# Kernel tuning notes

Hardware: AMD Instinct MI355X
Metric: run time of the kernel (lower is better)

Reference implementation:

```python
import math
import jax, jax.numpy as jnp
import numpy as np

D_MODEL = 1024
NUM_HEADS = 16
D_HEAD = D_MODEL // NUM_HEADS  # 64
K_S = 32  # sparse top-k keys kept per query
B, N = 2, 2048


def setup_inputs() -> dict:
    key = jax.random.key(0)
    ks = jax.random.split(key, 9)
    s = 1.0 / math.sqrt(D_MODEL)
    return {
        "x": jax.random.normal(ks[0], (B, N, D_MODEL), dtype=jnp.float32),
        "Wq": jax.random.normal(ks[1], (D_MODEL, D_MODEL), dtype=jnp.float32) * s,
        "bq": jnp.zeros((D_MODEL,), dtype=jnp.float32),
        "Wk": jax.random.normal(ks[2], (D_MODEL, D_MODEL), dtype=jnp.float32) * s,
        "bk": jnp.zeros((D_MODEL,), dtype=jnp.float32),
        "Wv": jax.random.normal(ks[3], (D_MODEL, D_MODEL), dtype=jnp.float32) * s,
        "bv": jnp.zeros((D_MODEL,), dtype=jnp.float32),
        "Wo": jax.random.normal(ks[4], (D_MODEL, D_MODEL), dtype=jnp.float32) * s,
        "bo": jnp.zeros((D_MODEL,), dtype=jnp.float32),
    }


def _attn(x, Wq, bq, Wk, bk, Wv, bv, Wo, bo):
    b, n, _ = x.shape
    # projections (torch Linear: y = x W^T + b)
    q = (x @ Wq.T + bq).reshape(b, n, NUM_HEADS, D_HEAD).transpose(0, 2, 1, 3)
    k = (x @ Wk.T + bk).reshape(b, n, NUM_HEADS, D_HEAD).transpose(0, 2, 1, 3)
    v = (x @ Wv.T + bv).reshape(b, n, NUM_HEADS, D_HEAD).transpose(0, 2, 1, 3)
    # full scores [b, H, n, n]
    scores = jnp.einsum("bhqd,bhkd->bhqk", q, k) / math.sqrt(D_HEAD)
    # causal mask (triu above diagonal -> -inf)
    causal = jnp.triu(jnp.ones((n, n), dtype=bool), k=1)
    neg_inf = jnp.array(-jnp.inf, dtype=scores.dtype)
    scores = jnp.where(causal, neg_inf, scores)
    # sparse top-k: keep only K_S largest scores per query row
    vals, idx = jax.lax.top_k(scores, K_S)
    masked = jnp.full_like(scores, -jnp.inf)
    masked = jnp.put_along_axis(masked, idx, vals, axis=-1, inplace=False)
    attn = jax.nn.softmax(masked, axis=-1)  # dropout p=0.0 -> identity
    out = jnp.einsum("bhqk,bhkd->bhqd", attn, v)
    out = out.transpose(0, 2, 1, 3).reshape(b, n, D_MODEL)
    y = out @ Wo.T + bo
    return y, attn.mean(axis=1)


def reference(x, Wq, bq, Wk, bk, Wv, bv, Wo, bo):
    return _attn(x, Wq, bq, Wk, bk, Wv, bv, Wo, bo)
```

## Files before the change

### kernel.cpp

```cpp
#include <hip/hip_runtime.h>
#include <hip/hip_bf16.h>
#include <math.h>

#define BATCH   2
#define NTOK    2048
#define DMODEL  1024
#define HEADS   16
#define DHEAD   64
#define KSEL    32
#define MROWS   (BATCH * NTOK)
#define NBLK8   (NTOK / 8)
#define TPW     8

typedef short     bf16x8 __attribute__((ext_vector_type(8)));
typedef float     f32x4  __attribute__((ext_vector_type(4)));
typedef unsigned short ushort_t;
typedef unsigned long long u64;

#define GLOAD_LDS16(g, l) \
    __builtin_amdgcn_global_load_lds((const __attribute__((address_space(1))) void*)(g), \
                                     (__attribute__((address_space(3))) void*)(l), 16, 0, 0)

__device__ __forceinline__ ushort_t f2bf(float f) {
    unsigned u = __float_as_uint(f);
    unsigned r = (u + 0x7FFFu + ((u >> 16) & 1u)) >> 16;
    return (ushort_t)r;
}
__device__ __forceinline__ float bf2f(ushort_t h) {
    return __uint_as_float(((unsigned)h) << 16);
}

__global__ __launch_bounds__(256) void conv_split(const float* __restrict__ in,
                                                  ushort_t* __restrict__ hi,
                                                  ushort_t* __restrict__ lo, int n)
{
    const int i = (blockIdx.x * 256 + threadIdx.x) * 4;
    if (i + 3 < n) {
        const float4 v = *(const float4*)(in + i);
        ushort4 ph, pl;
        ph.x = f2bf(v.x); pl.x = f2bf(v.x - bf2f(ph.x));
        ph.y = f2bf(v.y); pl.y = f2bf(v.y - bf2f(ph.y));
        ph.z = f2bf(v.z); pl.z = f2bf(v.z - bf2f(ph.z));
        ph.w = f2bf(v.w); pl.w = f2bf(v.w - bf2f(ph.w));
        *(ushort4*)(hi + i) = ph;
        *(ushort4*)(lo + i) = pl;
    }
}

__global__ __launch_bounds__(256) void zero_fill(float* __restrict__ p, int n4)
{
    const int i = blockIdx.x * 256 + threadIdx.x;
    if (i < n4) ((float4*)p)[i] = (float4){0.f, 0.f, 0.f, 0.f};
}

__device__ __forceinline__ unsigned mono_key(float f) {
    const unsigned u = __float_as_uint(f);
    return (u ^ (unsigned)(((int)u >> 31) | 0x80000000)) + 1u;
}
__device__ __forceinline__ float unmono(unsigned m) {
    const unsigned u = m - 1u;
    return __uint_as_float(u ^ (unsigned)(((int)(~u) >> 31) | 0x80000000));
}

__global__ __launch_bounds__(256, 2) void gemm_split_mfma(const ushort_t* __restrict__ Ahi,
                                                          const ushort_t* __restrict__ Alo,
                                                          const ushort_t* __restrict__ Bhi,
                                                          const ushort_t* __restrict__ Blo,
                                                          const float* __restrict__ bias,
                                                          float* __restrict__ out,
                                                          ushort_t* __restrict__ oh,
                                                          ushort_t* __restrict__ om,
                                                          ushort_t* __restrict__ ol,
                                                          int mode)
{
    __shared__ ushort_t smem[2 * 12288];

    const int tid  = threadIdx.x;
    const int wave = tid >> 6;
    const int lane = tid & 63;
    const int fr   = lane & 15;
    const int k8   = lane >> 4;
    const int m0 = blockIdx.x * 128;
    const int n0 = blockIdx.y * 64;

    f32x4 acc[2][4];
#pragma unroll
    for (int i = 0; i < 2; ++i)
#pragma unroll
        for (int j = 0; j < 4; ++j) acc[i][j] = (f32x4){0.f, 0.f, 0.f, 0.f};

#define STAGE(bufsel, k0v) do {                                                \
        ushort_t* dst_ = smem + (bufsel) * 12288;                              \
        _Pragma("unroll")                                                      \
        for (int i_ = 0; i_ < 2; ++i_) {                                       \
            const int c_ = i_ * 256 + tid;                                     \
            const int row_ = c_ >> 2;                                          \
            const int g_ = (c_ & 3) ^ ((row_ >> 1) & 3);                       \
            const size_t ga_ = (size_t)(m0 + row_) * DMODEL + (k0v) + g_ * 8;  \
            GLOAD_LDS16(Ahi + ga_, dst_ + (size_t)c_ * 8);                     \
            GLOAD_LDS16(Alo + ga_, dst_ + 4096 + (size_t)c_ * 8);              \
        }                                                                      \
        {                                                                      \
            const int c_ = tid;                                                \
            const int row_ = c_ >> 2;                                          \
            const int g_ = (c_ & 3) ^ ((row_ >> 1) & 3);                       \
            const size_t gb_ = (size_t)(n0 + row_) * DMODEL + (k0v) + g_ * 8;  \
            GLOAD_LDS16(Bhi + gb_, dst_ + 8192 + (size_t)c_ * 8);              \
            GLOAD_LDS16(Blo + gb_, dst_ + 10240 + (size_t)c_ * 8);             \
        }                                                                      \
    } while (0)

    STAGE(0, 0);
    int cur = 0;

    for (int k0 = 0; k0 < DMODEL; k0 += 32) {
        __syncthreads();
        if (k0 + 32 < DMODEL) STAGE(cur ^ 1, k0 + 32);

        const ushort_t* buf = smem + cur * 12288;
        bf16x8 afh[2], afl[2], bfh[4], bfl[4];
#pragma unroll
        for (int mi = 0; mi < 2; ++mi) {
            const int r = wave * 32 + mi * 16 + fr;
            const int ro = r * 32 + (k8 ^ ((r >> 1) & 3)) * 8;
            afh[mi] = *(const bf16x8*)(buf + ro);
            afl[mi] = *(const bf16x8*)(buf + 4096 + ro);
        }
#pragma unroll
        for (int ni = 0; ni < 4; ++ni) {
            const int r = ni * 16 + fr;
            const int ro = r * 32 + (k8 ^ ((r >> 1) & 3)) * 8;
            bfh[ni] = *(const bf16x8*)(buf + 8192 + ro);
            bfl[ni] = *(const bf16x8*)(buf + 10240 + ro);
        }

#pragma unroll
        for (int mi = 0; mi < 2; ++mi)
#pragma unroll
            for (int ni = 0; ni < 4; ++ni) {
                acc[mi][ni] = __builtin_amdgcn_mfma_f32_16x16x32_bf16(afh[mi], bfl[ni], acc[mi][ni], 0, 0, 0);
                acc[mi][ni] = __builtin_amdgcn_mfma_f32_16x16x32_bf16(afl[mi], bfh[ni], acc[mi][ni], 0, 0, 0);
                acc[mi][ni] = __builtin_amdgcn_mfma_f32_16x16x32_bf16(afh[mi], bfh[ni], acc[mi][ni], 0, 0, 0);
            }
        cur ^= 1;
    }
#undef STAGE

#pragma unroll
    for (int ni = 0; ni < 4; ++ni) {
        const int o = n0 + ni * 16 + (lane & 15);
        const float bv = bias[o];
#pragma unroll
        for (int mi = 0; mi < 2; ++mi) {
#pragma unroll
            for (int reg = 0; reg < 4; ++reg) {
                const int m = m0 + wave * 32 + mi * 16 + ((lane >> 4) << 2) + reg;
                const float v = acc[mi][ni][reg] + bv;
                if (mode == 0) {
                    out[(size_t)m * DMODEL + o] = v;
                } else {
                    const int bb = m >> 11;
                    const int n  = m & 2047;
                    const int hd = o >> 6;
                    const int d  = o & 63;
                    const size_t off = (((size_t)(bb * HEADS + hd)) * NTOK + n) * DHEAD + d;
                    if (mode == 1) {
                        out[off] = v;
                    } else {
                        const ushort_t h1 = f2bf(v);
                        const float r1 = v - bf2f(h1);
                        const ushort_t m1 = f2bf(r1);
                        const ushort_t l1 = f2bf(r1 - bf2f(m1));
                        oh[off] = h1; om[off] = m1; ol[off] = l1;
                    }
                }
            }
        }
    }
}

__global__ __launch_bounds__(256, 3) void score_mfma(const ushort_t* __restrict__ Qh,
                                                     const ushort_t* __restrict__ Qm,
                                                     const ushort_t* __restrict__ Ql,
                                                     const ushort_t* __restrict__ Kh,
                                                     const ushort_t* __restrict__ Km,
                                                     const ushort_t* __restrict__ Kl,
                                                     unsigned* __restrict__ S,
                                                     unsigned* __restrict__ Smax,
                                                     int q0, int QC)
{
    const int ks = blockIdx.x;
    const int qt = blockIdx.y;
    const int bh = blockIdx.z;
    const int qbase = q0 + qt * 128;
    const int ktmax = ((qbase + 127) >> 6) + 1;
    const int kt0 = ks * TPW;
    if (kt0 >= ktmax) return;
    const int kt1 = (kt0 + TPW < ktmax) ? (kt0 + TPW) : ktmax;

    __shared__ ushort_t smem[24576];

    const int tid  = threadIdx.x;
    const int wave = tid >> 6;
    const int lane = tid & 63;
    const int l15  = lane & 15;
    const int l4   = lane >> 4;

    const size_t qgbase = ((size_t)bh * NTOK + qbase) * DHEAD;

    {
        const ushort_t* Qp0 = Qh; const ushort_t* Qp1 = Qm; const ushort_t* Qp2 = Ql;
#pragma unroll
        for (int i = 0; i < 4; ++i) {
            const int c = i * 256 + tid;
            const int row = c >> 3;
            const int g = (c & 7) ^ (row & 7);
            const size_t goff = qgbase + (size_t)row * DHEAD + g * 8;
            GLOAD_LDS16(Qp0 + goff, smem + 0 * 8192 + (size_t)c * 8);
            GLOAD_LDS16(Qp1 + goff, smem + 1 * 8192 + (size_t)c * 8);
            GLOAD_LDS16(Qp2 + goff, smem + 2 * 8192 + (size_t)c * 8);
        }
    }
    __syncthreads();

    bf16x8 qf[3][2][2];
#pragma unroll
    for (int p = 0; p < 3; ++p)
#pragma unroll
        for (int j = 0; j < 2; ++j) {
            const int r = wave * 32 + j * 16 + l15;
#pragma unroll
            for (int h = 0; h < 2; ++h) {
                const int slot = (h * 4 + l4) ^ (r & 7);
                qf[p][j][h] = *(const bf16x8*)(smem + p * 8192 + (size_t)(r * 8 + slot) * 8);
            }
        }
    __syncthreads();

#define STAGE_K(bufsel, ktv) do {                                              \
        const size_t kg_ = ((size_t)bh * NTOK + (ktv) * 64) * DHEAD;           \
        _Pragma("unroll")                                                      \
        for (int i_ = 0; i_ < 2; ++i_) {                                       \
            const int c_ = i_ * 256 + tid;                                     \
            const int row_ = c_ >> 3;                                          \
            const int g_ = (c_ & 7) ^ (row_ & 7);                              \
            const size_t goff_ = kg_ + (size_t)row_ * DHEAD + g_ * 8;          \
            ushort_t* dst_ = smem + (bufsel) * 12288 + (size_t)c_ * 8;         \
            GLOAD_LDS16(Kh + goff_, dst_ + 0 * 4096);                          \
            GLOAD_LDS16(Km + goff_, dst_ + 1 * 4096);                          \
            GLOAD_LDS16(Kl + goff_, dst_ + 2 * 4096);                          \
        }                                                                      \
    } while (0)

    STAGE_K(0, kt0);
    int cur = 0;

    const size_t srowQ = (size_t)bh * QC;

    for (int kt = kt0; kt < kt1; ++kt) {
        __syncthreads();
        if (kt + 1 < kt1) STAGE_K(cur ^ 1, kt + 1);

        f32x4 acc[4][2];
#pragma unroll
        for (int m = 0; m < 4; ++m)
#pragma unroll
            for (int j = 0; j < 2; ++j) acc[m][j] = (f32x4){0.f, 0.f, 0.f, 0.f};

        const ushort_t* kb = smem + cur * 12288;
#pragma unroll
        for (int h = 0; h < 2; ++h) {
            bf16x8 kf[4];
#pragma unroll
            for (int m = 0; m < 4; ++m) {
                const int r = m * 16 + l15;
                const int slot = (h * 4 + l4) ^ (r & 7);
                kf[m] = *(const bf16x8*)(kb + 0 * 4096 + (size_t)(r * 8 + slot) * 8);
            }
#pragma unroll
            for (int m = 0; m < 4; ++m)
#pragma unroll
                for (int j = 0; j < 2; ++j) {
                    acc[m][j] = __builtin_amdgcn_mfma_f32_16x16x32_bf16(kf[m], qf[2][j][h], acc[m][j], 0, 0, 0);
                    acc[m][j] = __builtin_amdgcn_mfma_f32_16x16x32_bf16(kf[m], qf[1][j][h], acc[m][j], 0, 0, 0);
                    acc[m][j] = __builtin_amdgcn_mfma_f32_16x16x32_bf16(kf[m], qf[0][j][h], acc[m][j], 0, 0, 0);
                }
#pragma unroll
            for (int m = 0; m < 4; ++m) {
                const int r = m * 16 + l15;
                const int slot = (h * 4 + l4) ^ (r & 7);
                kf[m] = *(const bf16x8*)(kb + 1 * 4096 + (size_t)(r * 8 + slot) * 8);
            }
#pragma unroll
            for (int m = 0; m < 4; ++m)
#pragma unroll
                for (int j = 0; j < 2; ++j) {
                    acc[m][j] = __builtin_amdgcn_mfma_f32_16x16x32_bf16(kf[m], qf[1][j][h], acc[m][j], 0, 0, 0);
                    acc[m][j] = __builtin_amdgcn_mfma_f32_16x16x32_bf16(kf[m], qf[0][j][h], acc[m][j], 0, 0, 0);
                }
#pragma unroll
            for (int m = 0; m < 4; ++m) {
                const int r = m * 16 + l15;
                const int slot = (h * 4 + l4) ^ (r & 7);
                kf[m] = *(const bf16x8*)(kb + 2 * 4096 + (size_t)(r * 8 + slot) * 8);
            }
#pragma unroll
            for (int m = 0; m < 4; ++m)
#pragma unroll
                for (int j = 0; j < 2; ++j)
                    acc[m][j] = __builtin_amdgcn_mfma_f32_16x16x32_bf16(kf[m], qf[0][j][h], acc[m][j], 0, 0, 0);
        }

#pragma unroll
        for (int j = 0; j < 2; ++j) {
            const int qrow  = wave * 32 + j * 16 + l15;
            const int qlrow = qt * 128 + qrow;
            const int qglob = qbase + qrow;
            const size_t srow = (srowQ + qlrow) * NTOK;
            const size_t mrow = (srowQ + qlrow) * NBLK8;
#pragma unroll
            for (int m = 0; m < 4; ++m) {
                const int kcol0 = kt * 64 + m * 16 + (l4 << 2);
                uint4 kv;
                kv.x = mono_key(acc[m][j][0] * 0.125f);
                kv.y = mono_key(acc[m][j][1] * 0.125f);
                kv.z = mono_key(acc[m][j][2] * 0.125f);
                kv.w = mono_key(acc[m][j][3] * 0.125f);
                *(uint4*)(S + srow + kcol0) = kv;
                unsigned cm = (kcol0     <= qglob) ? kv.x : 0u;
                unsigned t;
                t = (kcol0 + 1 <= qglob) ? kv.y : 0u; cm = (t > cm) ? t : cm;
                t = (kcol0 + 2 <= qglob) ? kv.z : 0u; cm = (t > cm) ? t : cm;
                t = (kcol0 + 3 <= qglob) ? kv.w : 0u; cm = (t > cm) ? t : cm;
                const unsigned o = __shfl_xor(cm, 16, 64);
                cm = (o > cm) ? o : cm;
                if ((lane & 16) == 0) {
                    const int gblk = kt * 8 + m * 2 + (lane >> 5);
                    Smax[mrow + gblk] = cm;
                }
            }
        }
        cur ^= 1;
    }
#undef STAGE_K
}

__global__ __launch_bounds__(256) void select_v6(const unsigned* __restrict__ S,
                                                 const unsigned* __restrict__ Smax,
                                                 const float* __restrict__ V,
                                                 float* __restrict__ ctx,
                                                 float* __restrict__ attn,
                                                 int q0, int QC)
{
    __shared__ int   sBlkAll[4][KSEL];
    __shared__ int   sIdxAll[4][KSEL];
    __shared__ float sEAll[4][KSEL];

    const int lane = threadIdx.x & 63;
    const int wave = threadIdx.x >> 6;
    const int ql = blockIdx.x;
    const int b  = blockIdx.y >> 2;
    const int hg = blockIdx.y & 3;
    const int h  = hg * 4 + wave;
    const int q  = q0 + ql;
    const int L  = q + 1;
    const int nsel = (L < KSEL) ? L : KSEL;
    const int nb = (L + 7) >> 3;

    const size_t bhx = (size_t)(b * HEADS + h);
    const unsigned* Srow = S + (bhx * QC + ql) * NTOK;
    const unsigned* Mrow = Smax + (bhx * QC + ql) * NBLK8;
    const float* Vb   = V + bhx * NTOK * DHEAD;
    float* ctxRow  = ctx + (((size_t)(b * NTOK + q)) * HEADS + h) * DHEAD;
    float* attnRow = attn + ((size_t)(b * NTOK + q)) * NTOK;
    int*   sBlk = sBlkAll[wave];
    int*   sIdx = sIdxAll[wave];
    float* sE   = sEAll[wave];

    const uint4 bm4 = *(const uint4*)(Mrow + lane * 4);
    unsigned bmax[4] = {bm4.x, bm4.y, bm4.z, bm4.w};
#pragma unroll
    for (int s = 0; s < 4; ++s)
        if (lane * 4 + s >= nb) bmax[s] = 0u;

    unsigned gmax = bmax[0];
    gmax = (bmax[1] > gmax) ? bmax[1] : gmax;
    gmax = (bmax[2] > gmax) ? bmax[2] : gmax;
    gmax = (bmax[3] > gmax) ? bmax[3] : gmax;
#pragma unroll
    for (int d = 1; d < 64; d <<= 1) {
        const unsigned o = __shfl_xor(gmax, d, 64);
        gmax = (o > gmax) ? o : gmax;
    }
    const float vmax = unmono(gmax);

    unsigned selb = 0u;
    unsigned blkLo = 1u;
    int nselb;
    if (nb <= KSEL) {
        nselb = nb;
#pragma unroll
        for (int s = 0; s < 4; ++s)
            if (lane * 4 + s < nb) selb |= 1u << s;
    } else {
        nselb = KSEL;
        unsigned lo = 1u, hi = gmax >> 16;
        while (lo < hi) {
            const unsigned mid = lo + ((hi - lo + 1u) >> 1);
            const unsigned midk = mid << 16;
            int cnt = 0;
#pragma unroll
            for (int s = 0; s < 4; ++s)
                cnt += __popcll(__ballot(bmax[s] >= midk));
            if (cnt >= KSEL) lo = mid; else hi = mid - 1u;
        }
        blkLo = lo;
        const unsigned Tkb = lo << 16;
        const unsigned Gkb = Tkb | 0xFFFFu;
        int cge = 0, cgt = 0;
#pragma unroll
        for (int s = 0; s < 4; ++s) {
            cge += __popcll(__ballot(bmax[s] >= Tkb));
            cgt += __popcll(__ballot(bmax[s] > Gkb));
        }
        if (cge == KSEL) {
#pragma unroll
            for (int s = 0; s < 4; ++s)
                selb |= (bmax[s] >= Tkb) ? (1u << s) : 0u;
        } else {
            unsigned bmb = 0u;
#pragma unroll
            for (int s = 0; s < 4; ++s) {
                selb |= (bmax[s] > Gkb) ? (1u << s) : 0u;
                bmb  |= (bmax[s] >= Tkb && bmax[s] <= Gkb) ? (1u << s) : 0u;
            }
            int k_tie = KSEL - cgt;
            while (k_tie > 0) {
                u64 best = 0;
                unsigned bmm = bmb;
                while (bmm) {
                    const int s = __builtin_ctz(bmm);
                    bmm &= bmm - 1u;
                    const unsigned gblk = (unsigned)(lane * 4 + s);
                    const u64 k = ((u64)bmax[s] << 32) | (unsigned)~gblk;
                    if (k > best) best = k;
                }
                u64 bb = best;
#pragma unroll
                for (int d = 1; d < 64; d <<= 1) {
                    const u64 o = __shfl_xor(bb, d, 64);
                    bb = (o > bb) ? o : bb;
                }
                const unsigned gblk = ~(unsigned)bb;
                if (lane == (int)(gblk >> 2)) {
                    const unsigned bit = 1u << (gblk & 3u);
                    selb |= bit;
                    bmb &= ~bit;
                }
                --k_tie;
            }
        }
    }

    {
        const int cb = __popc(selb);
        int pfxb = cb;
#pragma unroll
        for (int d = 1; d < 64; d <<= 1) {
            const int t = __shfl_up(pfxb, d, 64);
            if (lane >= d) pfxb += t;
        }
        pfxb -= cb;
        unsigned mskb = selb;
        int posb = pfxb;
        while (mskb) {
            const int s = __builtin_ctz(mskb);
            mskb &= mskb - 1u;
            sBlk[posb++] = lane * 4 + s;
        }
    }
    __asm volatile("s_waitcnt lgkmcnt(0)" ::: "memory");

    const int NC = nselb * 8;
    unsigned km[4];
    int idx[4];
#pragma unroll
    for (int c = 0; c < 4; ++c) {
        const int t = c * 64 + lane;
        unsigned m = 0u;
        int j = 0;
        if (t < NC) {
            const int blk = sBlk[t >> 3];
            j = blk * 8 + (t & 7);
            if (j < L) m = Srow[j];
        }
        km[c] = m;
        idx[c] = j;
    }

    unsigned lo = blkLo, hi = gmax >> 16;
    while (lo < hi) {
        const unsigned mid = lo + ((hi - lo + 1u) >> 1);
        const unsigned midk = mid << 16;
        int cnt = 0;
#pragma unroll
        for (int c = 0; c < 4; ++c)
            cnt += __popcll(__ballot(km[c] >= midk));
        if (cnt >= nsel) lo = mid; else hi = mid - 1u;
    }
    const unsigned Tk = lo << 16;
    const unsigned Gk = Tk | 0xFFFFu;

    int cnt_ge = 0, cnt_gt = 0;
#pragma unroll
    for (int c = 0; c < 4; ++c) {
        cnt_ge += __popcll(__ballot(km[c] >= Tk));
        cnt_gt += __popcll(__ballot(km[c] > Gk));
    }

    unsigned selmask = 0u;
    if (cnt_ge == nsel) {
#pragma unroll
        for (int c = 0; c < 4; ++c)
            selmask |= (km[c] >= Tk) ? (1u << c) : 0u;
    } else {
        unsigned bmask = 0u;
#pragma unroll
        for (int c = 0; c < 4; ++c) {
            selmask |= (km[c] > Gk) ? (1u << c) : 0u;
            bmask   |= (km[c] >= Tk && km[c] <= Gk) ? (1u << c) : 0u;
        }
        int k_tie = nsel - cnt_gt;
        while (k_tie > 0) {
            u64 best = 0;
            unsigned bmm = bmask;
            while (bmm) {
                const int c = __builtin_ctz(bmm);
                bmm &= bmm - 1u;
                const int t = c * 64 + lane;
                const u64 k = ((u64)km[c] << 32) |
                              ((u64)(0xFFFFu ^ (unsigned)idx[c]) << 16) | (u64)t;
                if (k > best) best = k;
            }
            u64 bb = best;
#pragma unroll
            for (int d = 1; d < 64; d <<= 1) {
                const u64 o = __shfl_xor(bb, d, 64);
                bb = (o > bb) ? o : bb;
            }
            const unsigned tt = (unsigned)bb & 0xFFFFu;
            if (lane == (int)(tt & 63u)) {
                const unsigned bit = 1u << (tt >> 6);
                selmask |= bit;
                bmask &= ~bit;
            }
            --k_tie;
        }
    }

    const int csel = __popc(selmask);
    int pfx = csel;
#pragma unroll
    for (int d = 1; d < 64; d <<= 1) {
        const int t = __shfl_up(pfx, d, 64);
        if (lane >= d) pfx += t;
    }
    pfx -= csel;

    float esum = 0.f;
    unsigned msk = selmask;
    int pos = pfx;
    while (msk) {
        const int c = __builtin_ctz(msk);
        msk &= msk - 1u;
        const float e = __expf(unmono(km[c]) - vmax);
        esum += e;
        sIdx[pos] = idx[c];
        sE[pos] = e;
        ++pos;
    }

    float Z = esum;
#pragma unroll
    for (int d = 1; d < 64; d <<= 1) Z += __shfl_xor(Z, d, 64);
    const float rcpZ = 1.0f / Z;

    msk = selmask;
    pos = pfx;
    while (msk) {
        const int c = __builtin_ctz(msk);
        msk &= msk - 1u;
        const float w = sE[pos] * rcpZ;
        ++pos;
        atomicAdd(&attnRow[idx[c]], w * (1.0f / (float)HEADS));
    }

    float acc = 0.f;
    for (int i = 0; i < nsel; ++i) {
        const int id = sIdx[i];
        const float wi = sE[i] * rcpZ;
        acc += wi * Vb[(size_t)id * DHEAD + lane];
    }
    ctxRow[lane] = acc;
}

extern "C" void kernel_launch(void* const* d_in, const int* in_sizes, int n_in,
                              void* d_out, int out_size, void* d_ws, size_t ws_size,
                              hipStream_t stream) {
    const float* x  = (const float*)d_in[0];
    const float* Wq = (const float*)d_in[1];
    const float* bq = (const float*)d_in[2];
    const float* Wk = (const float*)d_in[3];
    const float* bk = (const float*)d_in[4];
    const float* Wv = (const float*)d_in[5];
    const float* bv = (const float*)d_in[6];
    const float* Wo = (const float*)d_in[7];
    const float* bo = (const float*)d_in[8];

    const size_t MB = 1ull << 20;
    char* wsb = (char*)d_ws;
    float*    Vws = (float*)(wsb + 0 * MB);
    float*    ctx = (float*)(wsb + 16 * MB);
    ushort_t* xhi = (ushort_t*)(wsb + 32 * MB);
    ushort_t* xlo = (ushort_t*)(wsb + 40 * MB);
    ushort_t* wqh = (ushort_t*)(wsb + 48 * MB);
    ushort_t* wql = (ushort_t*)(wsb + 50 * MB);
    ushort_t* wkh = (ushort_t*)(wsb + 52 * MB);
    ushort_t* wkl = (ushort_t*)(wsb + 54 * MB);
    ushort_t* wvh = (ushort_t*)(wsb + 56 * MB);
    ushort_t* wvl = (ushort_t*)(wsb + 58 * MB);
    ushort_t* woh = (ushort_t*)(wsb + 60 * MB);
    ushort_t* wol = (ushort_t*)(wsb + 62 * MB);
    ushort_t* Qh  = (ushort_t*)(wsb + 64 * MB);
    ushort_t* Qm  = (ushort_t*)(wsb + 72 * MB);
    ushort_t* Ql  = (ushort_t*)(wsb + 80 * MB);
    ushort_t* Kh  = (ushort_t*)(wsb + 88 * MB);
    ushort_t* Km  = (ushort_t*)(wsb + 96 * MB);
    ushort_t* Kl  = (ushort_t*)(wsb + 104 * MB);
    ushort_t* cxh = xhi;
    ushort_t* cxl = xlo;

    float* y    = (float*)d_out;
    float* attn = y + (size_t)BATCH * NTOK * DMODEL;

    const int NX = MROWS * DMODEL;
    const int NW = DMODEL * DMODEL;

    conv_split<<<NX / (256 * 4), 256, 0, stream>>>(x, xhi, xlo, NX);
    conv_split<<<NW / (256 * 4), 256, 0, stream>>>(Wq, wqh, wql, NW);
    conv_split<<<NW / (256 * 4), 256, 0, stream>>>(Wk, wkh, wkl, NW);
    conv_split<<<NW / (256 * 4), 256, 0, stream>>>(Wv, wvh, wvl, NW);
    conv_split<<<NW / (256 * 4), 256, 0, stream>>>(Wo, woh, wol, NW);

    dim3 ggrid(MROWS / 128, DMODEL / 64);
    gemm_split_mfma<<<ggrid, 256, 0, stream>>>(xhi, xlo, wqh, wql, bq, nullptr, Qh, Qm, Ql, 2);
    gemm_split_mfma<<<ggrid, 256, 0, stream>>>(xhi, xlo, wkh, wkl, bk, nullptr, Kh, Km, Kl, 2);
    gemm_split_mfma<<<ggrid, 256, 0, stream>>>(xhi, xlo, wvh, wvl, bv, Vws, nullptr, nullptr, nullptr, 1);

    const size_t base_bytes = 112 * MB;
    const size_t avail = (ws_size > base_bytes) ? ws_size - base_bytes : 0;
    int QC = 128;
    for (int cand = NTOK; cand >= 128; cand >>= 1) {
        const size_t need = (size_t)BATCH * HEADS * cand * (size_t)(NTOK + NBLK8) * sizeof(unsigned);
        if (need <= avail) { QC = cand; break; }
    }
    unsigned* Smax = (unsigned*)(wsb + base_bytes);
    unsigned* Sws  = (unsigned*)(wsb + base_bytes +
                                 (size_t)BATCH * HEADS * QC * NBLK8 * sizeof(unsigned));

    const int nattn4 = BATCH * NTOK * NTOK / 4;
    zero_fill<<<(nattn4 + 255) / 256, 256, 0, stream>>>(attn, nattn4);
    for (int q0 = 0; q0 < NTOK; q0 += QC) {
        const int ktm = (q0 + QC) >> 6;
        dim3 sgrid((ktm + TPW - 1) / TPW, QC / 128, BATCH * HEADS);
        score_mfma<<<sgrid, 256, 0, stream>>>(Qh, Qm, Ql, Kh, Km, Kl, Sws, Smax, q0, QC);
        dim3 selgrid(QC, BATCH * 4);
        select_v6<<<selgrid, 256, 0, stream>>>(Sws, Smax, Vws, ctx, attn, q0, QC);
    }

    conv_split<<<NX / (256 * 4), 256, 0, stream>>>(ctx, cxh, cxl, NX);
    gemm_split_mfma<<<ggrid, 256, 0, stream>>>(cxh, cxl, woh, wol, bo, y, nullptr, nullptr, nullptr, 0);
}
```

Before: 549.5 us.

## Batch weight conversions, raise GEMM occupancy, and streamline score-kernel K pipeline

```diff
diff --git a/kernel.cpp b/kernel.cpp
--- a/kernel.cpp
+++ b/kernel.cpp
@@ -30,11 +30,10 @@
     return __uint_as_float(((unsigned)h) << 16);
 }
 
-__global__ __launch_bounds__(256) void conv_split(const float* __restrict__ in,
-                                                  ushort_t* __restrict__ hi,
-                                                  ushort_t* __restrict__ lo, int n)
+__device__ __forceinline__ void conv_body(const float* __restrict__ in,
+                                          ushort_t* __restrict__ hi,
+                                          ushort_t* __restrict__ lo, int n, int i)
 {
-    const int i = (blockIdx.x * 256 + threadIdx.x) * 4;
     if (i + 3 < n) {
         const float4 v = *(const float4*)(in + i);
         ushort4 ph, pl;
@@ -47,6 +46,28 @@
     }
 }
 
+__global__ __launch_bounds__(256) void conv_split(const float* __restrict__ in,
+                                                  ushort_t* __restrict__ hi,
+                                                  ushort_t* __restrict__ lo, int n)
+{
+    const int i = (blockIdx.x * 256 + threadIdx.x) * 4;
+    conv_body(in, hi, lo, n, i);
+}
+
+__global__ __launch_bounds__(256) void conv_split4(const float* __restrict__ i0, ushort_t* __restrict__ h0, ushort_t* __restrict__ l0,
+                                                   const float* __restrict__ i1, ushort_t* __restrict__ h1, ushort_t* __restrict__ l1,
+                                                   const float* __restrict__ i2, ushort_t* __restrict__ h2, ushort_t* __restrict__ l2,
+                                                   const float* __restrict__ i3, ushort_t* __restrict__ h3, ushort_t* __restrict__ l3,
+                                                   int n)
+{
+    const int w = blockIdx.y;
+    const float* in = (w == 0) ? i0 : (w == 1) ? i1 : (w == 2) ? i2 : i3;
+    ushort_t* hi = (w == 0) ? h0 : (w == 1) ? h1 : (w == 2) ? h2 : h3;
+    ushort_t* lo = (w == 0) ? l0 : (w == 1) ? l1 : (w == 2) ? l2 : l3;
+    const int i = (blockIdx.x * 256 + threadIdx.x) * 4;
+    conv_body(in, hi, lo, n, i);
+}
+
 __global__ __launch_bounds__(256) void zero_fill(float* __restrict__ p, int n4)
 {
     const int i = blockIdx.x * 256 + threadIdx.x;
@@ -62,7 +83,7 @@
     return __uint_as_float(u ^ (unsigned)(((int)(~u) >> 31) | 0x80000000));
 }
 
-__global__ __launch_bounds__(256, 2) void gemm_split_mfma(const ushort_t* __restrict__ Ahi,
+__global__ __launch_bounds__(256, 3) void gemm_split_mfma(const ushort_t* __restrict__ Ahi,
                                                           const ushort_t* __restrict__ Alo,
                                                           const ushort_t* __restrict__ Bhi,
                                                           const ushort_t* __restrict__ Blo,
@@ -198,7 +219,7 @@
     if (kt0 >= ktmax) return;
     const int kt1 = (kt0 + TPW < ktmax) ? (kt0 + TPW) : ktmax;
 
-    __shared__ ushort_t smem[24576];
+    __shared__ ushort_t smem[2 * 12288];
 
     const int tid  = threadIdx.x;
     const int wave = tid >> 6;
@@ -208,34 +229,18 @@
 
     const size_t qgbase = ((size_t)bh * NTOK + qbase) * DHEAD;
 
-    {
-        const ushort_t* Qp0 = Qh; const ushort_t* Qp1 = Qm; const ushort_t* Qp2 = Ql;
-#pragma unroll
-        for (int i = 0; i < 4; ++i) {
-            const int c = i * 256 + tid;
-            const int row = c >> 3;
-            const int g = (c & 7) ^ (row & 7);
-            const size_t goff = qgbase + (size_t)row * DHEAD + g * 8;
-            GLOAD_LDS16(Qp0 + goff, smem + 0 * 8192 + (size_t)c * 8);
-            GLOAD_LDS16(Qp1 + goff, smem + 1 * 8192 + (size_t)c * 8);
-            GLOAD_LDS16(Qp2 + goff, smem + 2 * 8192 + (size_t)c * 8);
-        }
-    }
-    __syncthreads();
-
     bf16x8 qf[3][2][2];
 #pragma unroll
-    for (int p = 0; p < 3; ++p)
+    for (int p = 0; p < 3; ++p) {
+        const ushort_t* Qp = (p == 0) ? Qh : (p == 1) ? Qm : Ql;
 #pragma unroll
         for (int j = 0; j < 2; ++j) {
             const int r = wave * 32 + j * 16 + l15;
 #pragma unroll
-            for (int h = 0; h < 2; ++h) {
-                const int slot = (h * 4 + l4) ^ (r & 7);
-                qf[p][j][h] = *(const bf16x8*)(smem + p * 8192 + (size_t)(r * 8 + slot) * 8);
-            }
-        }
-    __syncthreads();
+            for (int h = 0; h < 2; ++h)
+                qf[p][j][h] = *(const bf16x8*)(Qp + qgbase + (size_t)r * DHEAD + (h * 4 + l4) * 8);
+        }
+    }
 
 #define STAGE_K(bufsel, ktv) do {                                              \
         const size_t kg_ = ((size_t)bh * NTOK + (ktv) * 64) * DHEAD;           \
@@ -253,13 +258,18 @@
     } while (0)
 
     STAGE_K(0, kt0);
+    __builtin_amdgcn_sched_barrier(0);
+    asm volatile("s_waitcnt vmcnt(0)" ::: "memory");
+    __builtin_amdgcn_s_barrier();
+    __builtin_amdgcn_sched_barrier(0);
+
     int cur = 0;
-
     const size_t srowQ = (size_t)bh * QC;
 
     for (int kt = kt0; kt < kt1; ++kt) {
-        __syncthreads();
-        if (kt + 1 < kt1) STAGE_K(cur ^ 1, kt + 1);
+        const bool more = (kt + 1 < kt1);
+        if (more) STAGE_K(cur ^ 1, kt + 1);
+        __builtin_amdgcn_sched_barrier(0);
 
         f32x4 acc[4][2];
 #pragma unroll
@@ -339,6 +349,12 @@
                     Smax[mrow + gblk] = cm;
                 }
             }
+        }
+
+        if (more) {
+            asm volatile("s_waitcnt vmcnt(16)" ::: "memory");
+            __builtin_amdgcn_s_barrier();
+            __builtin_amdgcn_sched_barrier(0);
         }
         cur ^= 1;
     }
@@ -647,10 +663,13 @@
     const int NW = DMODEL * DMODEL;
 
     conv_split<<<NX / (256 * 4), 256, 0, stream>>>(x, xhi, xlo, NX);
-    conv_split<<<NW / (256 * 4), 256, 0, stream>>>(Wq, wqh, wql, NW);
-    conv_split<<<NW / (256 * 4), 256, 0, stream>>>(Wk, wkh, wkl, NW);
-    conv_split<<<NW / (256 * 4), 256, 0, stream>>>(Wv, wvh, wvl, NW);
-    conv_split<<<NW / (256 * 4), 256, 0, stream>>>(Wo, woh, wol, NW);
+    {
+        dim3 cgrid(NW / (256 * 4), 4);
+        conv_split4<<<cgrid, 256, 0, stream>>>(Wq, wqh, wql,
+                                               Wk, wkh, wkl,
+                                               Wv, wvh, wvl,
+                                               Wo, woh, wol, NW);
+    }
 
     dim3 ggrid(MROWS / 128, DMODEL / 64);
     gemm_split_mfma<<<ggrid, 256, 0, stream>>>(xhi, xlo, wqh, wql, bq, nullptr, Qh, Qm, Ql, 2);
```

After: 534.7 us. 2.7% less time.
